# Optimization experiments

Measured on AMD Instinct MI355X. Metric: run time of the kernel, lower is better.

Reference implementation:

```python
import jax, jax.numpy as jnp
import numpy as np

B, NA, NB = 2, 2048, 2048
DIM_A, DIM_B = 256, 256
HEADS, DH_A, DH_B = 8, 64, 64
INNER_A, INNER_B = DH_A * HEADS, DH_B * HEADS
EPS = 1e-5


def layer_norm(x, w, b):
    m = jnp.mean(x, axis=-1, keepdims=True)
    v = jnp.mean(jnp.square(x - m), axis=-1, keepdims=True)
    return (x - m) * jax.lax.rsqrt(v + EPS) * w + b


def setup_inputs() -> dict:
    key = jax.random.key(0)
    ks = jax.random.split(key, 16)
    s = 0.02
    return {
        "feat_a": jax.random.normal(ks[0], (B, NA, DIM_A), jnp.float32),
        "feat_b": jax.random.normal(ks[1], (B, NB, DIM_B), jnp.float32),
        "mask_a_b": jax.random.bernoulli(ks[2], 0.5, (B, NA, NB)),
        # linear weights stored (in, out)
        "Wq": jax.random.normal(ks[3], (DIM_A, INNER_B), jnp.float32) * s,
        "bq": jnp.zeros((INNER_B,), jnp.float32),
        "Wk": jax.random.normal(ks[4], (DIM_B, INNER_B), jnp.float32) * s,
        "bk": jnp.zeros((INNER_B,), jnp.float32),
        "Wv": jax.random.normal(ks[5], (DIM_B, INNER_A), jnp.float32) * s,
        "bv": jnp.zeros((INNER_A,), jnp.float32),
        "Wg": jax.random.normal(ks[6], (DIM_A, INNER_A), jnp.float32) * s,
        "bg": jnp.zeros((INNER_A,), jnp.float32),
        "Wo": jax.random.normal(ks[7], (INNER_A, DIM_A), jnp.float32) * s,
        "bo": jnp.zeros((DIM_A,), jnp.float32),
        "ln_a_w": jnp.ones((DIM_A,), jnp.float32),
        "ln_a_b": jnp.zeros((DIM_A,), jnp.float32),
        "ln_b_w": jnp.ones((DIM_B,), jnp.float32),
        "ln_b_b": jnp.zeros((DIM_B,), jnp.float32),
        "qln_w": jnp.ones((INNER_B,), jnp.float32),
        "qln_b": jnp.zeros((INNER_B,), jnp.float32),
        "kln_w": jnp.ones((INNER_B,), jnp.float32),
        "kln_b": jnp.zeros((INNER_B,), jnp.float32),
    }


def reference(feat_a, feat_b, mask_a_b, Wq, bq, Wk, bk, Wv, bv, Wg, bg, Wo, bo,
              ln_a_w, ln_a_b, ln_b_w, ln_b_b, qln_w, qln_b, kln_w, kln_b):
    scale = DH_B ** -0.5
    fa = layer_norm(feat_a, ln_a_w, ln_a_b)            # (b, na, dim_a)
    fb = layer_norm(feat_b, ln_b_w, ln_b_b)            # (b, nb, dim_b)
    q = layer_norm(fa @ Wq + bq, qln_w, qln_b)         # (b, na, inner_b)
    k = layer_norm(fb @ Wk + bk, kln_w, kln_b)         # (b, nb, inner_b)
    v = fb @ Wv + bv                                   # (b, nb, inner_a)
    g = fa @ Wg + bg                                   # (b, na, inner_a)
    q = q.reshape(B, NA, HEADS, DH_B)
    k = k.reshape(B, NB, HEADS, DH_B)
    v = v.reshape(B, NB, HEADS, DH_A)
    g = g.reshape(B, NA, HEADS, DH_A)
    sim = jnp.einsum('bihd,bjhd->bhij', q, k) * scale  # (b, h, na, nb)
    neg = jnp.finfo(sim.dtype).min
    sim = jnp.where(mask_a_b[:, None, :, :], sim, neg)
    attn = jax.nn.softmax(sim, axis=-1)
    out = jnp.einsum('bhij,bjhd->bihd', attn, v)       # (b, na, h, dh_a)
    out = jax.nn.sigmoid(g) * out
    out = out.reshape(B, NA, INNER_A)
    return out @ Wo + bo                               # (b, na, dim_a)
```

## Files before the change

### kernel.cpp

```cpp
#include <hip/hip_runtime.h>
#include <hip/hip_bf16.h>

using bf16 = __hip_bfloat16;
typedef short bf16x8 __attribute__((ext_vector_type(8)));
typedef float f32x4 __attribute__((ext_vector_type(4)));
typedef unsigned short ushort8_t __attribute__((ext_vector_type(8)));
typedef unsigned uint4_t __attribute__((ext_vector_type(4)));
typedef unsigned uint2_t __attribute__((ext_vector_type(2)));
typedef unsigned long long u64;

static constexpr int NA_ = 2048, NB_ = 2048;
static constexpr int H_ = 8, DH_ = 64, INNER_ = 512;
static constexpr int MROWS = 2 * NA_;

#define MFMA32(a, b, c) __builtin_amdgcn_mfma_f32_16x16x32_bf16(a, b, c, 0, 0, 0)

#if __has_builtin(__builtin_amdgcn_exp2f)
#define EXP2(x) __builtin_amdgcn_exp2f(x)
#else
#define EXP2(x) exp2f(x)
#endif

__device__ __forceinline__ unsigned short bfbits(float x) {
  bf16 h = __float2bfloat16(x);
  return __builtin_bit_cast(unsigned short, h);
}
__device__ __forceinline__ float b2f(unsigned short u) {
  unsigned v = ((unsigned)u) << 16;
  return __builtin_bit_cast(float, v);
}

__device__ __forceinline__ unsigned pkbf(float a, float b) {
  unsigned ua = __builtin_bit_cast(unsigned, a) + 0x8000u;
  unsigned ub = __builtin_bit_cast(unsigned, b) + 0x8000u;
#if __has_builtin(__builtin_amdgcn_perm)
  return __builtin_amdgcn_perm(ub, ua, 0x07060302u);
#else
  return (ua >> 16) | (ub & 0xFFFF0000u);
#endif
}

__global__ __launch_bounds__(256) void prep_kernel(
    const float* __restrict__ fa_in, const float* __restrict__ fb_in,
    const float* __restrict__ law, const float* __restrict__ lab,
    const float* __restrict__ lbw, const float* __restrict__ lbb,
    bf16* __restrict__ fa, bf16* __restrict__ fb,
    const float* __restrict__ Wq, const float* __restrict__ Wk,
    const float* __restrict__ Wv, const float* __restrict__ Wg,
    const float* __restrict__ Wo,
    bf16* __restrict__ Wqt, bf16* __restrict__ Wkt,
    bf16* __restrict__ Wvt, bf16* __restrict__ Wgt,
    bf16* __restrict__ Woth, bf16* __restrict__ Wotl,
    const void* __restrict__ maskp, u64* __restrict__ mbits) {
  int blk = blockIdx.x;
  int t = threadIdx.x;
  if (blk < 2048) {
    int row = blk * 4 + (t >> 6);
    int lane = t & 63;
    const float *src, *w, *bb;
    bf16* dst;
    int r;
    if (row < MROWS) { src = fa_in; w = law; bb = lab; dst = fa; r = row; }
    else             { src = fb_in; w = lbw; bb = lbb; dst = fb; r = row - MROWS; }
    float4 x = *(const float4*)(src + (size_t)r * 256 + lane * 4);
    float s  = (x.x + x.y) + (x.z + x.w);
    float s2 = (x.x * x.x + x.y * x.y) + (x.z * x.z + x.w * x.w);
#pragma unroll
    for (int m = 32; m >= 1; m >>= 1) { s += __shfl_xor(s, m); s2 += __shfl_xor(s2, m); }
    float mean = s * (1.0f / 256.0f);
    float var  = s2 * (1.0f / 256.0f) - mean * mean;
    float rstd = rsqrtf(var + 1e-5f);
    float4 wv = *(const float4*)(w + lane * 4);
    float4 bv = *(const float4*)(bb + lane * 4);
    ushort4 o;
    o.x = bfbits((x.x - mean) * rstd * wv.x + bv.x);
    o.y = bfbits((x.y - mean) * rstd * wv.y + bv.y);
    o.z = bfbits((x.z - mean) * rstd * wv.z + bv.z);
    o.w = bfbits((x.w - mean) * rstd * wv.w + bv.w);
    *(ushort4*)(dst + (size_t)r * 256 + lane * 4) = o;
  } else if (blk < 4608) {
    int z = (blk - 2048) >> 9;
    int idx = ((blk - 2048) & 511) * 256 + t;
    if (z < 4) {
      const float* W = (z == 0) ? Wq : (z == 1) ? Wk : (z == 2) ? Wv : Wg;
      bf16* Wt = (z == 0) ? Wqt : (z == 1) ? Wkt : (z == 2) ? Wvt : Wgt;
      int kk = idx >> 9, n = idx & 511;
      Wt[n * 256 + kk] = __float2bfloat16(W[idx]);
    } else {
      int kk = idx >> 8, n = idx & 255;
      float w = Wo[idx];
      bf16 hi = __float2bfloat16(w);
      Woth[n * 512 + kk] = hi;
      Wotl[n * 512 + kk] = __float2bfloat16(w - __bfloat162float(hi));
    }
  } else {
    __shared__ unsigned shf[4];
    const unsigned char* mu = (const unsigned char*)maskp;
    bool nz = ((t & 3) != 0) && (mu[t] != 0);
    u64 bal = __ballot(nz);
    if ((t & 63) == 0) shf[t >> 6] = (bal != 0ull) ? 1u : 0u;
    __syncthreads();
    bool m8 = (shf[0] | shf[1] | shf[2] | shf[3]) != 0;
    int lane = t & 63, wid = t >> 6;
    int lb = blk - 4608;
    for (size_t word = (size_t)lb * 4 + wid; word < 131072; word += 8192) {
      size_t e = word * 64 + lane;
      int v = m8 ? (int)mu[e] : ((const int*)maskp)[e];
      u64 b2 = __ballot(v != 0);
      if (lane == 0) mbits[word] = b2;
    }
  }
}

__global__ __launch_bounds__(256) void gemm4_kernel(
    const bf16* __restrict__ fa, const bf16* __restrict__ fb,
    const bf16* __restrict__ Wqt, const bf16* __restrict__ Wkt,
    const bf16* __restrict__ Wgt, const bf16* __restrict__ Wvt,
    const float* __restrict__ bq, const float* __restrict__ bk,
    const float* __restrict__ bg, const float* __restrict__ bv,
    const float* __restrict__ qlw, const float* __restrict__ qlb,
    const float* __restrict__ klw, const float* __restrict__ klb,
    bf16* __restrict__ qo, bf16* __restrict__ ko,
    bf16* __restrict__ gout, bf16* __restrict__ vout) {
  __shared__ __align__(16) char sm[27648];
  int z = blockIdx.z;
  int t = threadIdx.x, wave = t >> 6, lane = t & 63;
  int lm = lane & 15, quad = lane >> 4, q8 = quad * 8;

// ... 130 lines not shown
        for (int ni = 0; ni < 4; ni++) {
          int nn = n0 + ni * 16 + lm;
          float bvv = bias[nn];
          int mb = m0 + wm + mi * 16 + quad * 4;
#pragma unroll
          for (int r = 0; r < 4; r++)
            gout[(size_t)(mb + r) * 512 + nn] = __float2bfloat16(acc[mi][ni][r] + bvv);
        }
    } else {
      __syncthreads();
      bf16* buf = (bf16*)sm;
#pragma unroll
      for (int mi = 0; mi < 2; mi++)
#pragma unroll
        for (int ni = 0; ni < 4; ni++) {
          int d_local = ni * 16 + lm;
          float bvv = bias[n0 + d_local];
          int j_local = wm + mi * 16 + quad * 4;
#pragma unroll
          for (int r = 0; r < 4; r++)
            buf[d_local * 136 + j_local + r] = __float2bfloat16(acc[mi][ni][r] + bvv);
        }
      __syncthreads();
      int bidx2 = m0 >> 11, j0g = m0 & 2047, hh = n0 >> 6;
      int dl = t >> 2, jseg = (t & 3) * 32;
      bf16* dstrow = vout + (size_t)((bidx2 * 8 + hh) * 64 + dl) * 2048 + j0g + jseg;
#pragma unroll
      for (int c = 0; c < 4; c++)
        *(ushort8_t*)(dstrow + c * 8) = *(const ushort8_t*)(&buf[dl * 136 + jseg + c * 8]);
    }
  }
}

__global__ __launch_bounds__(512, 4) void attn_kernel(
    const bf16* __restrict__ q, const bf16* __restrict__ k,
    const bf16* __restrict__ vt, const bf16* __restrict__ g,
    const u64* __restrict__ mbits,
    bf16* __restrict__ gh, bf16* __restrict__ gl) {
  __shared__ __align__(16) char smem[46592];
  bf16* Qs = (bf16*)smem;
  bf16* KVB = (bf16*)(smem + 9216);
  float* Om = (float*)(smem + 9216);
  float* Lbuf = (float*)(smem + 46080);
  constexpr int BUFE = 2 * 64 * 72;

  int flat = blockIdx.y * 32 + blockIdx.x;
  int bh = (flat & 7) * 2 + (flat >> 8);
  int qt = (flat >> 3) & 31;
  int bidx = bh >> 3, h = bh & 7;
  int i0 = qt * 64;
  int t = threadIdx.x, wave = t >> 6, lane = t & 63;
  int wj = wave >> 2, wi = wave & 3;
  int lm = lane & 15, quad = lane >> 4, q8 = quad * 8;
  int wj32 = wj * 32, wi16 = wi * 16;
  int srow = t >> 3, scg = (t & 7) * 8;

  int sg = srow & 31;
  int ksrow = (srow & 32) + (((sg & 4) << 2) | ((sg & 24) >> 1) | (sg & 3));
  int ksl = ksrow * 72 + scg;
  int vsl = srow * 72 + scg;

  const bf16* kb = k + (size_t)(bidx * NB_) * INNER_ + h * DH_;
  const bf16* vb = vt + (size_t)(bh * DH_) * NB_;
  const bf16* ksrc = kb + (size_t)srow * INNER_ + scg;
  const bf16* vsrc = vb + (size_t)srow * NB_ + scg;

  *(ushort8_t*)(&Qs[srow * 72 + scg]) =
      *(const ushort8_t*)(q + (size_t)(bidx * NA_ + i0 + srow) * INNER_ + h * DH_ + scg);

  ushort8_t kr = *(const ushort8_t*)(ksrc);
  ushort8_t vr = *(const ushort8_t*)(vsrc);

  __syncthreads();
  bf16x8 bq0 = *(const bf16x8*)(&Qs[(wi16 + lm) * 72 + q8]);
  bf16x8 bq1 = *(const bf16x8*)(&Qs[(wi16 + lm) * 72 + 32 + q8]);

  *(ushort8_t*)(&KVB[ksl]) = kr;
  *(ushort8_t*)(&KVB[64 * 72 + vsl]) = vr;
  kr = *(const ushort8_t*)(ksrc + 64 * INNER_);
  vr = *(const ushort8_t*)(vsrc + 64);

  bf16x8 bone;
  {
    short onev = (lm == 0) ? (short)0x3F80 : (short)0;
#pragma unroll
    for (int i = 0; i < 8; i++) bone[i] = onev;
  }

  f32x4 oacc[4] = {};
  f32x4 lacc = {};

  const u64* mrp = mbits + (size_t)(bidx * NA_ + i0 + wi16 + lm) * (NB_ / 64);
  int shp = wj32 + quad * 8;
  u64 smw = mrp[0] >> shp;

  __syncthreads();

  for (int it = 0; it < 32; it++) {
    bf16* Ks = KVB + (it & 1) * BUFE;
    bf16* Vs = Ks + 64 * 72;
    if (it < 31) {
      bf16* Kn = KVB + ((it + 1) & 1) * BUFE;
      *(ushort8_t*)(&Kn[ksl]) = kr;
      *(ushort8_t*)(&Kn[64 * 72 + vsl]) = vr;
    }
    if (it < 30) {
      kr = *(const ushort8_t*)(ksrc + (size_t)(it + 2) * (64 * INNER_));
      vr = *(const ushort8_t*)(vsrc + (it + 2) * 64);
    }
    u64 nm = (it < 31) ? (mrp[it + 1] >> shp) : 0;

    bf16x8 a00 = *(const bf16x8*)(&Ks[(wj32 + lm) * 72 + q8]);
    bf16x8 a01 = *(const bf16x8*)(&Ks[(wj32 + lm) * 72 + 32 + q8]);
    bf16x8 a10 = *(const bf16x8*)(&Ks[(wj32 + 16 + lm) * 72 + q8]);
    bf16x8 a11 = *(const bf16x8*)(&Ks[(wj32 + 16 + lm) * 72 + 32 + q8]);
    f32x4 st0 = {0.f, 0.f, 0.f, 0.f}, st1 = {0.f, 0.f, 0.f, 0.f};
    st0 = MFMA32(a00, bq0, st0);
    st0 = MFMA32(a01, bq1, st0);
    st1 = MFMA32(a10, bq0, st1);
    st1 = MFMA32(a11, bq1, st1);

    float p0[4], p1[4];
#pragma unroll
    for (int r = 0; r < 4; r++) {
      bool l0 = (smw >> r) & 1ull;
      bool l1 = (smw >> (4 + r)) & 1ull;
      p0[r] = EXP2(l0 ? st0[r] : -200.0f);
      p1[r] = EXP2(l1 ? st1[r] : -200.0f);
    }

    uint4_t u0;
    u0[0] = pkbf(p0[0], p0[1]);
    u0[1] = pkbf(p0[2], p0[3]);
    u0[2] = pkbf(p1[0], p1[1]);
    u0[3] = pkbf(p1[2], p1[3]);
    bf16x8 pa = __builtin_bit_cast(bf16x8, u0);

#pragma unroll
    for (int c = 0; c < 4; c++) {
      bf16x8 v_ = *(const bf16x8*)(&Vs[(c * 16 + lm) * 72 + wj32 + q8]);
      oacc[c] = MFMA32(pa, v_, oacc[c]);
    }
    lacc = MFMA32(pa, bone, lacc);

    smw = nm;
    __syncthreads();
  }

  if (lm == 0) {
#pragma unroll
    for (int r = 0; r < 4; r++)
      Lbuf[wj * 64 + wi16 + quad * 4 + r] = lacc[r];
  }
  if (wj == 1) {
#pragma unroll
    for (int c = 0; c < 4; c++)
#pragma unroll
      for (int r = 0; r < 4; r++)
        Om[(wi16 + quad * 4 + r) * 66 + c * 16 + lm] = oacc[c][r];
  }
  __syncthreads();
  if (wj == 0) {
#pragma unroll
    for (int c = 0; c < 4; c++)
#pragma unroll
      for (int r = 0; r < 4; r++)
        Om[(wi16 + quad * 4 + r) * 66 + c * 16 + lm] += oacc[c][r];
  }
  __syncthreads();
  {
    int row = wave * 8 + (lane >> 3);
    int col = (lane & 7) * 8;
    float l = Lbuf[row] + Lbuf[64 + row];
    float inv = 1.0f / l;
    size_t idx = (size_t)(bidx * NA_ + i0 + row) * INNER_ + h * DH_ + col;
    ushort8_t gv = *(const ushort8_t*)(g + idx);
    ushort8_t oh, ol;
#pragma unroll
    for (int e = 0; e < 8; e++) {
      float o = Om[row * 66 + col + e];
      float gf = b2f((unsigned short)gv[e]);
      float sig = 1.0f / (1.0f + __expf(-gf));
      float val = o * inv * sig;
      unsigned short hb = bfbits(val);
      oh[e] = hb;
      ol[e] = bfbits(val - b2f(hb));
    }
    *(ushort8_t*)(gh + idx) = oh;
    *(ushort8_t*)(gl + idx) = ol;
  }
}

__global__ __launch_bounds__(256) void gemm_split_kernel(
    const bf16* __restrict__ Ah, const bf16* __restrict__ Al,
    const bf16* __restrict__ Bh, const bf16* __restrict__ Bl,
    const float* __restrict__ bias, float* __restrict__ C) {
  constexpr int K = 512, N = 256;
  __shared__ __align__(16) bf16 Ash[32 * 72];
  __shared__ __align__(16) bf16 Asl[32 * 72];
  __shared__ __align__(16) bf16 Bsh[64 * 72];
  __shared__ __align__(16) bf16 Bsl[64 * 72];
  int n0 = blockIdx.x * 64, m0 = blockIdx.y * 32;
  int t = threadIdx.x, wave = t >> 6, lane = t & 63;
  int lm = lane & 15, quad = lane >> 4, q8 = quad * 8;
  int wm = (wave & 1) * 16, wn = (wave >> 1) * 32;
  f32x4 acc[2] = {};
  for (int k0 = 0; k0 < K; k0 += 64) {
    __syncthreads();
    {
      int r = t >> 3, cg = t & 7;
      size_t ga = (size_t)(m0 + r) * K + k0 + cg * 8;
      *(ushort8_t*)(&Ash[r * 72 + cg * 8]) = *(const ushort8_t*)(Ah + ga);
      *(ushort8_t*)(&Asl[r * 72 + cg * 8]) = *(const ushort8_t*)(Al + ga);
    }
#pragma unroll
    for (int i = 0; i < 2; i++) {
      int id = t + 256 * i, r = id >> 3, cg = id & 7;
      size_t gb = (size_t)(n0 + r) * K + k0 + cg * 8;
      *(ushort8_t*)(&Bsh[r * 72 + cg * 8]) = *(const ushort8_t*)(Bh + gb);
      *(ushort8_t*)(&Bsl[r * 72 + cg * 8]) = *(const ushort8_t*)(Bl + gb);
    }
    __syncthreads();
// ... 38 lines not shown
  const float* Wo = (const float*)d_in[11];
  const float* bo = (const float*)d_in[12];
  const float* law = (const float*)d_in[13];
  const float* lab = (const float*)d_in[14];
  const float* lbw = (const float*)d_in[15];
  const float* lbb = (const float*)d_in[16];
  const float* qlw = (const float*)d_in[17];
  const float* qlb = (const float*)d_in[18];
  const float* klw = (const float*)d_in[19];
  const float* klb = (const float*)d_in[20];

  char* ws = (char*)d_ws;
  size_t off = 0;
  auto alloc = [&](size_t bytes) -> void* {
    void* p = ws + off;
    off += (bytes + 255) & ~(size_t)255;
    return p;
  };
  bf16* fa    = (bf16*)alloc((size_t)MROWS * 256 * 2);
  bf16* fb    = (bf16*)alloc((size_t)MROWS * 256 * 2);
  bf16* Wqt   = (bf16*)alloc((size_t)131072 * 2);
  bf16* Wkt   = (bf16*)alloc((size_t)131072 * 2);
  bf16* Wvt   = (bf16*)alloc((size_t)131072 * 2);
  bf16* Wgt   = (bf16*)alloc((size_t)131072 * 2);
  bf16* Woth  = (bf16*)alloc((size_t)131072 * 2);
  bf16* Wotl  = (bf16*)alloc((size_t)131072 * 2);
  bf16* qb_   = (bf16*)alloc((size_t)MROWS * 512 * 2);
  bf16* kb_   = (bf16*)alloc((size_t)MROWS * 512 * 2);
  bf16* vtb   = (bf16*)alloc((size_t)1024 * 2048 * 2);
  bf16* gbuf  = (bf16*)alloc((size_t)MROWS * 512 * 2);
  bf16* gh    = (bf16*)alloc((size_t)MROWS * 512 * 2);
  bf16* gl    = (bf16*)alloc((size_t)MROWS * 512 * 2);
  u64*  mbits = (u64*)alloc((size_t)131072 * 8);

  prep_kernel<<<6656, 256, 0, stream>>>(
      feat_a, feat_b, law, lab, lbw, lbb, fa, fb,
      Wq, Wk, Wv, Wg, Wo, Wqt, Wkt, Wvt, Wgt, Woth, Wotl, mask, mbits);
  gemm4_kernel<<<dim3(256, 1, 4), 256, 0, stream>>>(
      fa, fb, Wqt, Wkt, Wgt, Wvt, bq, bk, bg, bv,
      qlw, qlb, klw, klb, qb_, kb_, gbuf, vtb);
  attn_kernel<<<dim3(32, 16), 512, 0, stream>>>(qb_, kb_, vtb, gbuf, mbits, gh, gl);
  gemm_split_kernel<<<dim3(4, 128), 256, 0, stream>>>(gh, gl, Woth, Wotl, bo, (float*)d_out);
}
```

Measured before the change: 189.2 us.

## Split attention over key halves with flag-based partial combine

The attention kernel now splits the key/value range into two halves across a third grid dimension, doubling the block count. Each block drops from 8 to 4 waves, and every wave now covers 32 query rows instead of 16, which reuses each K/V fragment across two row tiles. Each block writes partial O and L sums to global scratch and bumps an atomic counter per (head, query tile). The block that arrives second combines both halves and applies the gate and bf16 hi/lo split. This aims for more parallelism and better register reuse, at the cost of extra global traffic, a threadfence-based handoff, and flags that the prep kernel must reset on every launch.

```diff
diff --git a/kernel.cpp b/kernel.cpp
--- a/kernel.cpp
+++ b/kernel.cpp
@@ -6,7 +6,6 @@
 typedef float f32x4 __attribute__((ext_vector_type(4)));
 typedef unsigned short ushort8_t __attribute__((ext_vector_type(8)));
 typedef unsigned uint4_t __attribute__((ext_vector_type(4)));
-typedef unsigned uint2_t __attribute__((ext_vector_type(2)));
 typedef unsigned long long u64;
 
 static constexpr int NA_ = 2048, NB_ = 2048;
@@ -51,7 +50,8 @@
     bf16* __restrict__ Wqt, bf16* __restrict__ Wkt,
     bf16* __restrict__ Wvt, bf16* __restrict__ Wgt,
     bf16* __restrict__ Woth, bf16* __restrict__ Wotl,
-    const void* __restrict__ maskp, u64* __restrict__ mbits) {
+    const void* __restrict__ maskp, u64* __restrict__ mbits,
+    unsigned* __restrict__ flags) {
   int blk = blockIdx.x;
   int t = threadIdx.x;
   if (blk < 2048) {
@@ -94,6 +94,7 @@
       Wotl[n * 512 + kk] = __float2bfloat16(w - __bfloat162float(hi));
     }
   } else {
+    if (blk - 4608 < 2) flags[(blk - 4608) * 256 + t] = 0u;
     __shared__ unsigned shf[4];
     const unsigned char* mu = (const unsigned char*)maskp;
     bool nz = ((t & 3) != 0) && (mu[t] != 0);
@@ -290,53 +291,51 @@
   }
 }
 
-__global__ __launch_bounds__(512, 4) void attn_kernel(
+__global__ __launch_bounds__(256, 4) void attn_kernel(
     const bf16* __restrict__ q, const bf16* __restrict__ k,
     const bf16* __restrict__ vt, const bf16* __restrict__ g,
     const u64* __restrict__ mbits,
+    float* __restrict__ opart, float* __restrict__ lpart,
+    unsigned* __restrict__ flags,
     bf16* __restrict__ gh, bf16* __restrict__ gl) {
-  __shared__ __align__(16) char smem[46592];
-  bf16* Qs = (bf16*)smem;
-  bf16* KVB = (bf16*)(smem + 9216);
-  float* Om = (float*)(smem + 9216);
-  float* Lbuf = (float*)(smem + 46080);
+  __shared__ __align__(16) char smem[37408];
+  bf16* KVB = (bf16*)smem;
+  float* Om = (float*)smem;
+  float* Lbuf = (float*)(smem + 36864);
+  unsigned* sflag = (unsigned*)(smem + 37376);
   constexpr int BUFE = 2 * 64 * 72;
 
-  int flat = blockIdx.y * 32 + blockIdx.x;
-  int bh = (flat & 7) * 2 + (flat >> 8);
-  int qt = (flat >> 3) & 31;
+  int fid = blockIdx.x + 32 * blockIdx.y + 512 * blockIdx.z;
+  int bh = (fid & 7) * 2 + ((fid >> 3) & 1);
+  int qt = (fid >> 4) & 31;
+  int jh = fid >> 9;
   int bidx = bh >> 3, h = bh & 7;
   int i0 = qt * 64;
+  int pair = bh * 32 + qt;
   int t = threadIdx.x, wave = t >> 6, lane = t & 63;
-  int wj = wave >> 2, wi = wave & 3;
+  int wj = wave >> 1, wi = wave & 1;
   int lm = lane & 15, quad = lane >> 4, q8 = quad * 8;
-  int wj32 = wj * 32, wi16 = wi * 16;
+  int wj32 = wj * 32, wi32 = wi * 32;
   int srow = t >> 3, scg = (t & 7) * 8;
 
-  int sg = srow & 31;
-  int ksrow = (srow & 32) + (((sg & 4) << 2) | ((sg & 24) >> 1) | (sg & 3));
-  int ksl = ksrow * 72 + scg;
-  int vsl = srow * 72 + scg;
+  int ksrow = ((srow & 4) << 2) | ((srow & 24) >> 1) | (srow & 3);
+  int ksl0 = ksrow * 72 + scg;
+  int ksl1 = (ksrow + 32) * 72 + scg;
+  int vsl0 = srow * 72 + scg;
+  int vsl1 = (srow + 32) * 72 + scg;
 
   const bf16* kb = k + (size_t)(bidx * NB_) * INNER_ + h * DH_;
   const bf16* vb = vt + (size_t)(bh * DH_) * NB_;
-  const bf16* ksrc = kb + (size_t)srow * INNER_ + scg;
-  const bf16* vsrc = vb + (size_t)srow * NB_ + scg;
-
-  *(ushort8_t*)(&Qs[srow * 72 + scg]) =
-      *(const ushort8_t*)(q + (size_t)(bidx * NA_ + i0 + srow) * INNER_ + h * DH_ + scg);
-
-  ushort8_t kr = *(const ushort8_t*)(ksrc);
-  ushort8_t vr = *(const ushort8_t*)(vsrc);
-
-  __syncthreads();
-  bf16x8 bq0 = *(const bf16x8*)(&Qs[(wi16 + lm) * 72 + q8]);
-  bf16x8 bq1 = *(const bf16x8*)(&Qs[(wi16 + lm) * 72 + 32 + q8]);
-
-  *(ushort8_t*)(&KVB[ksl]) = kr;
-  *(ushort8_t*)(&KVB[64 * 72 + vsl]) = vr;
-  kr = *(const ushort8_t*)(ksrc + 64 * INNER_);
-  vr = *(const ushort8_t*)(vsrc + 64);
+  const bf16* ksrc0 = kb + (size_t)(jh * 1024 + srow) * INNER_ + scg;
+  const bf16* ksrc1 = kb + (size_t)(jh * 1024 + srow + 32) * INNER_ + scg;
+  const bf16* vsrc0 = vb + (size_t)srow * NB_ + jh * 1024 + scg;
+  const bf16* vsrc1 = vb + (size_t)(srow + 32) * NB_ + jh * 1024 + scg;
+
+  const bf16* qbase = q + (size_t)(bidx * NA_ + i0 + wi32 + lm) * INNER_ + h * DH_;
+  bf16x8 bq00 = *(const bf16x8*)(qbase + q8);
+  bf16x8 bq01 = *(const bf16x8*)(qbase + 32 + q8);
+  bf16x8 bq10 = *(const bf16x8*)(qbase + 16 * INNER_ + q8);
+  bf16x8 bq11 = *(const bf16x8*)(qbase + 16 * INNER_ + 32 + q8);
 
   bf16x8 bone;
   {
@@ -345,107 +344,177 @@
     for (int i = 0; i < 8; i++) bone[i] = onev;
   }
 
-  f32x4 oacc[4] = {};
-  f32x4 lacc = {};
-
-  const u64* mrp = mbits + (size_t)(bidx * NA_ + i0 + wi16 + lm) * (NB_ / 64);
+  f32x4 oacc[2][4] = {};
+  f32x4 lacc[2] = {};
+
+  const u64* mrp0 = mbits + (size_t)(bidx * NA_ + i0 + wi32 + lm) * (NB_ / 64) + jh * 16;
+  const u64* mrp1 = mrp0 + (size_t)16 * (NB_ / 64);
   int shp = wj32 + quad * 8;
-  u64 smw = mrp[0] >> shp;
-
+
+  ushort8_t kr0 = *(const ushort8_t*)(ksrc0);
+  ushort8_t kr1 = *(const ushort8_t*)(ksrc1);
+  ushort8_t vr0 = *(const ushort8_t*)(vsrc0);
+  ushort8_t vr1 = *(const ushort8_t*)(vsrc1);
+  *(ushort8_t*)(&KVB[ksl0]) = kr0;
+  *(ushort8_t*)(&KVB[ksl1]) = kr1;
+  *(ushort8_t*)(&KVB[64 * 72 + vsl0]) = vr0;
+  *(ushort8_t*)(&KVB[64 * 72 + vsl1]) = vr1;
+  kr0 = *(const ushort8_t*)(ksrc0 + 64 * INNER_);
+  kr1 = *(const ushort8_t*)(ksrc1 + 64 * INNER_);
+  vr0 = *(const ushort8_t*)(vsrc0 + 64);
+  vr1 = *(const ushort8_t*)(vsrc1 + 64);
+  u64 smw0 = mrp0[0] >> shp;
+  u64 smw1 = mrp1[0] >> shp;
   __syncthreads();
 
-  for (int it = 0; it < 32; it++) {
+  for (int it = 0; it < 16; it++) {
     bf16* Ks = KVB + (it & 1) * BUFE;
     bf16* Vs = Ks + 64 * 72;
-    if (it < 31) {
+    if (it < 15) {
       bf16* Kn = KVB + ((it + 1) & 1) * BUFE;
-      *(ushort8_t*)(&Kn[ksl]) = kr;
-      *(ushort8_t*)(&Kn[64 * 72 + vsl]) = vr;
-    }
-    if (it < 30) {
-      kr = *(const ushort8_t*)(ksrc + (size_t)(it + 2) * (64 * INNER_));
-      vr = *(const ushort8_t*)(vsrc + (it + 2) * 64);
-    }
-    u64 nm = (it < 31) ? (mrp[it + 1] >> shp) : 0;
+      *(ushort8_t*)(&Kn[ksl0]) = kr0;
+      *(ushort8_t*)(&Kn[ksl1]) = kr1;
+      *(ushort8_t*)(&Kn[64 * 72 + vsl0]) = vr0;
+      *(ushort8_t*)(&Kn[64 * 72 + vsl1]) = vr1;
+    }
+    if (it < 14) {
+      kr0 = *(const ushort8_t*)(ksrc0 + (size_t)(it + 2) * (64 * INNER_));
+      kr1 = *(const ushort8_t*)(ksrc1 + (size_t)(it + 2) * (64 * INNER_));
+      vr0 = *(const ushort8_t*)(vsrc0 + (it + 2) * 64);
+      vr1 = *(const ushort8_t*)(vsrc1 + (it + 2) * 64);
+    }
+    u64 nm0 = smw0, nm1 = smw1;
+    if (it < 15) {
+      nm0 = mrp0[it + 1] >> shp;
+      nm1 = mrp1[it + 1] >> shp;
+    }
 
     bf16x8 a00 = *(const bf16x8*)(&Ks[(wj32 + lm) * 72 + q8]);
     bf16x8 a01 = *(const bf16x8*)(&Ks[(wj32 + lm) * 72 + 32 + q8]);
     bf16x8 a10 = *(const bf16x8*)(&Ks[(wj32 + 16 + lm) * 72 + q8]);
     bf16x8 a11 = *(const bf16x8*)(&Ks[(wj32 + 16 + lm) * 72 + 32 + q8]);
-    f32x4 st0 = {0.f, 0.f, 0.f, 0.f}, st1 = {0.f, 0.f, 0.f, 0.f};
-    st0 = MFMA32(a00, bq0, st0);
-    st0 = MFMA32(a01, bq1, st0);
-    st1 = MFMA32(a10, bq0, st1);
-    st1 = MFMA32(a11, bq1, st1);
-
-    float p0[4], p1[4];
+    f32x4 st00 = {0.f, 0.f, 0.f, 0.f}, st01 = {0.f, 0.f, 0.f, 0.f};
+    f32x4 st10 = {0.f, 0.f, 0.f, 0.f}, st11 = {0.f, 0.f, 0.f, 0.f};
+    st00 = MFMA32(a00, bq00, st00); st00 = MFMA32(a01, bq01, st00);
+    st01 = MFMA32(a10, bq00, st01); st01 = MFMA32(a11, bq01, st01);
+    st10 = MFMA32(a00, bq10, st10); st10 = MFMA32(a01, bq11, st10);
+    st11 = MFMA32(a10, bq10, st11); st11 = MFMA32(a11, bq11, st11);
+
+    float p00[4], p01[4], p10[4], p11[4];
 #pragma unroll
     for (int r = 0; r < 4; r++) {
-      bool l0 = (smw >> r) & 1ull;
-      bool l1 = (smw >> (4 + r)) & 1ull;
-      p0[r] = EXP2(l0 ? st0[r] : -200.0f);
-      p1[r] = EXP2(l1 ? st1[r] : -200.0f);
-    }
-
-    uint4_t u0;
-    u0[0] = pkbf(p0[0], p0[1]);
-    u0[1] = pkbf(p0[2], p0[3]);
-    u0[2] = pkbf(p1[0], p1[1]);
-    u0[3] = pkbf(p1[2], p1[3]);
-    bf16x8 pa = __builtin_bit_cast(bf16x8, u0);
+      p00[r] = EXP2(((smw0 >> r) & 1ull) ? st00[r] : -200.0f);
+      p01[r] = EXP2(((smw0 >> (4 + r)) & 1ull) ? st01[r] : -200.0f);
+      p10[r] = EXP2(((smw1 >> r) & 1ull) ? st10[r] : -200.0f);
+      p11[r] = EXP2(((smw1 >> (4 + r)) & 1ull) ? st11[r] : -200.0f);
+    }
+
+    uint4_t u0, u1;
+    u0[0] = pkbf(p00[0], p00[1]);
+    u0[1] = pkbf(p00[2], p00[3]);
+    u0[2] = pkbf(p01[0], p01[1]);
+    u0[3] = pkbf(p01[2], p01[3]);
+    u1[0] = pkbf(p10[0], p10[1]);
+    u1[1] = pkbf(p10[2], p10[3]);
+    u1[2] = pkbf(p11[0], p11[1]);
+    u1[3] = pkbf(p11[2], p11[3]);
+    bf16x8 pa0 = __builtin_bit_cast(bf16x8, u0);
+    bf16x8 pa1 = __builtin_bit_cast(bf16x8, u1);
 
 #pragma unroll
     for (int c = 0; c < 4; c++) {
       bf16x8 v_ = *(const bf16x8*)(&Vs[(c * 16 + lm) * 72 + wj32 + q8]);
-      oacc[c] = MFMA32(pa, v_, oacc[c]);
-    }
-    lacc = MFMA32(pa, bone, lacc);
-
-    smw = nm;
+      oacc[0][c] = MFMA32(pa0, v_, oacc[0][c]);
+      oacc[1][c] = MFMA32(pa1, v_, oacc[1][c]);
+    }
+    lacc[0] = MFMA32(pa0, bone, lacc[0]);
+    lacc[1] = MFMA32(pa1, bone, lacc[1]);
+
+    smw0 = nm0;
+    smw1 = nm1;
     __syncthreads();
   }
 
   if (lm == 0) {
 #pragma unroll
-    for (int r = 0; r < 4; r++)
-      Lbuf[wj * 64 + wi16 + quad * 4 + r] = lacc[r];
+    for (int is_ = 0; is_ < 2; is_++)
+#pragma unroll
+      for (int r = 0; r < 4; r++)
+        Lbuf[wj * 64 + wi32 + is_ * 16 + quad * 4 + r] = lacc[is_][r];
   }
   if (wj == 1) {
 #pragma unroll
-    for (int c = 0; c < 4; c++)
-#pragma unroll
-      for (int r = 0; r < 4; r++)
-        Om[(wi16 + quad * 4 + r) * 66 + c * 16 + lm] = oacc[c][r];
+    for (int is_ = 0; is_ < 2; is_++)
+#pragma unroll
+      for (int c = 0; c < 4; c++)
+#pragma unroll
+        for (int r = 0; r < 4; r++)
+          Om[(wi32 + is_ * 16 + quad * 4 + r) * 66 + c * 16 + lm] = oacc[is_][c][r];
   }
   __syncthreads();
   if (wj == 0) {
 #pragma unroll
-    for (int c = 0; c < 4; c++)
-#pragma unroll
-      for (int r = 0; r < 4; r++)
-        Om[(wi16 + quad * 4 + r) * 66 + c * 16 + lm] += oacc[c][r];
+    for (int is_ = 0; is_ < 2; is_++)
+#pragma unroll
+      for (int c = 0; c < 4; c++)
+#pragma unroll
+        for (int r = 0; r < 4; r++)
+          Om[(wi32 + is_ * 16 + quad * 4 + r) * 66 + c * 16 + lm] += oacc[is_][c][r];
   }
   __syncthreads();
+
+  int slot = pair * 2 + jh;
   {
-    int row = wave * 8 + (lane >> 3);
-    int col = (lane & 7) * 8;
-    float l = Lbuf[row] + Lbuf[64 + row];
+    int row = t >> 2, c0 = (t & 3) * 16;
+    float* dst = opart + (size_t)slot * 4096 + row * 64 + c0;
+#pragma unroll
+    for (int e = 0; e < 4; e++) {
+      float4 v4 = *(float4*)(&Om[row * 66 + c0 + e * 4]);
+      *(float4*)(dst + e * 4) = v4;
+    }
+    if (t < 64) lpart[slot * 64 + t] = Lbuf[t] + Lbuf[64 + t];
+  }
+  __syncthreads();
+  __threadfence();
+  if (t == 0) *sflag = atomicAdd(&flags[pair], 1u);
+  __syncthreads();
+  if (*sflag == 0) return;
+  __threadfence();
+
+  {
+    int pslot = pair * 2 + (1 - jh);
+    int row = t >> 2, c0 = (t & 3) * 16;
+    const float* psrc = opart + (size_t)pslot * 4096 + row * 64 + c0;
+    float l = Lbuf[row] + Lbuf[64 + row] + lpart[pslot * 64 + row];
     float inv = 1.0f / l;
-    size_t idx = (size_t)(bidx * NA_ + i0 + row) * INNER_ + h * DH_ + col;
-    ushort8_t gv = *(const ushort8_t*)(g + idx);
-    ushort8_t oh, ol;
+    size_t idx = (size_t)(bidx * NA_ + i0 + row) * INNER_ + h * DH_ + c0;
+    ushort8_t gv0 = *(const ushort8_t*)(g + idx);
+    ushort8_t gv1 = *(const ushort8_t*)(g + idx + 8);
+    ushort8_t oh0, ol0, oh1, ol1;
 #pragma unroll
     for (int e = 0; e < 8; e++) {
-      float o = Om[row * 66 + col + e];
-      float gf = b2f((unsigned short)gv[e]);
+      float o = Om[row * 66 + c0 + e] + psrc[e];
+      float gf = b2f((unsigned short)gv0[e]);
       float sig = 1.0f / (1.0f + __expf(-gf));
       float val = o * inv * sig;
       unsigned short hb = bfbits(val);
-      oh[e] = hb;
-      ol[e] = bfbits(val - b2f(hb));
-    }
-    *(ushort8_t*)(gh + idx) = oh;
-    *(ushort8_t*)(gl + idx) = ol;
+      oh0[e] = hb;
+      ol0[e] = bfbits(val - b2f(hb));
+    }
+#pragma unroll
+    for (int e = 0; e < 8; e++) {
+      float o = Om[row * 66 + c0 + 8 + e] + psrc[8 + e];
+      float gf = b2f((unsigned short)gv1[e]);
+      float sig = 1.0f / (1.0f + __expf(-gf));
+      float val = o * inv * sig;
+      unsigned short hb = bfbits(val);
+      oh1[e] = hb;
+      ol1[e] = bfbits(val - b2f(hb));
+    }
+    *(ushort8_t*)(gh + idx) = oh0;
+    *(ushort8_t*)(gh + idx + 8) = oh1;
+    *(ushort8_t*)(gl + idx) = ol0;
+    *(ushort8_t*)(gl + idx + 8) = ol1;
   }
 }
 
@@ -550,13 +619,17 @@
   bf16* gh    = (bf16*)alloc((size_t)MROWS * 512 * 2);
   bf16* gl    = (bf16*)alloc((size_t)MROWS * 512 * 2);
   u64*  mbits = (u64*)alloc((size_t)131072 * 8);
+  float* opart = (float*)alloc((size_t)1024 * 4096 * 4);
+  float* lpart = (float*)alloc((size_t)1024 * 64 * 4);
+  unsigned* flags = (unsigned*)alloc((size_t)512 * 4);
 
   prep_kernel<<<6656, 256, 0, stream>>>(
       feat_a, feat_b, law, lab, lbw, lbb, fa, fb,
-      Wq, Wk, Wv, Wg, Wo, Wqt, Wkt, Wvt, Wgt, Woth, Wotl, mask, mbits);
+      Wq, Wk, Wv, Wg, Wo, Wqt, Wkt, Wvt, Wgt, Woth, Wotl, mask, mbits, flags);
   gemm4_kernel<<<dim3(256, 1, 4), 256, 0, stream>>>(
       fa, fb, Wqt, Wkt, Wgt, Wvt, bq, bk, bg, bv,
       qlw, qlb, klw, klb, qb_, kb_, gbuf, vtb);
-  attn_kernel<<<dim3(32, 16), 512, 0, stream>>>(qb_, kb_, vtb, gbuf, mbits, gh, gl);
+  attn_kernel<<<dim3(32, 16, 2), 256, 0, stream>>>(
+      qb_, kb_, vtb, gbuf, mbits, opart, lpart, flags, gh, gl);
   gemm_split_kernel<<<dim3(4, 128), 256, 0, stream>>>(gh, gl, Woth, Wotl, bo, (float*)d_out);
 }
```

New measurement: 397.4 us. 110% more time.

## Retile attention so each wave covers 32 query rows across two key-tile halves

Applied to the files above, without the earlier changes.

Each wave now handles two 16-row query blocks instead of one, reusing the same K and V fragments from shared memory for both. The 8 waves split into 2 query halves, 2 key halves and 2 key-tile groups, and each iteration stages two 64-key K/V tiles. This halves the loop trip count and the number of barriers, and Q fragments are now loaded straight from global into registers. In exchange, shared memory grows to about 73 KB, register pressure rises from the doubled accumulators, and the final reduction across four wave groups needs more serialized barrier steps. Occupancy per CU may drop.

```diff
diff --git a/kernel.cpp b/kernel.cpp
--- a/kernel.cpp
+++ b/kernel.cpp
@@ -6,7 +6,6 @@
 typedef float f32x4 __attribute__((ext_vector_type(4)));
 typedef unsigned short ushort8_t __attribute__((ext_vector_type(8)));
 typedef unsigned uint4_t __attribute__((ext_vector_type(4)));
-typedef unsigned uint2_t __attribute__((ext_vector_type(2)));
 typedef unsigned long long u64;
 
 static constexpr int NA_ = 2048, NB_ = 2048;
@@ -295,12 +294,12 @@
     const bf16* __restrict__ vt, const bf16* __restrict__ g,
     const u64* __restrict__ mbits,
     bf16* __restrict__ gh, bf16* __restrict__ gl) {
-  __shared__ __align__(16) char smem[46592];
-  bf16* Qs = (bf16*)smem;
-  bf16* KVB = (bf16*)(smem + 9216);
-  float* Om = (float*)(smem + 9216);
-  float* Lbuf = (float*)(smem + 46080);
-  constexpr int BUFE = 2 * 64 * 72;
+  __shared__ __align__(16) char smem[74752];
+  bf16* KVB = (bf16*)smem;
+  float* Om = (float*)smem;
+  float* Lbuf = (float*)(smem + 73728);
+  constexpr int TILE = 64 * 72;
+  constexpr int BUFE = 4 * TILE;
 
   int flat = blockIdx.y * 32 + blockIdx.x;
   int bh = (flat & 7) * 2 + (flat >> 8);
@@ -308,9 +307,9 @@
   int bidx = bh >> 3, h = bh & 7;
   int i0 = qt * 64;
   int t = threadIdx.x, wave = t >> 6, lane = t & 63;
-  int wj = wave >> 2, wi = wave & 3;
+  int wi = wave & 1, wj = (wave >> 1) & 1, jh = wave >> 2;
   int lm = lane & 15, quad = lane >> 4, q8 = quad * 8;
-  int wj32 = wj * 32, wi16 = wi * 16;
+  int wj32 = wj * 32, wi32 = wi * 32;
   int srow = t >> 3, scg = (t & 7) * 8;
 
   int sg = srow & 31;
@@ -323,20 +322,11 @@
   const bf16* ksrc = kb + (size_t)srow * INNER_ + scg;
   const bf16* vsrc = vb + (size_t)srow * NB_ + scg;
 
-  *(ushort8_t*)(&Qs[srow * 72 + scg]) =
-      *(const ushort8_t*)(q + (size_t)(bidx * NA_ + i0 + srow) * INNER_ + h * DH_ + scg);
-
-  ushort8_t kr = *(const ushort8_t*)(ksrc);
-  ushort8_t vr = *(const ushort8_t*)(vsrc);
-
-  __syncthreads();
-  bf16x8 bq0 = *(const bf16x8*)(&Qs[(wi16 + lm) * 72 + q8]);
-  bf16x8 bq1 = *(const bf16x8*)(&Qs[(wi16 + lm) * 72 + 32 + q8]);
-
-  *(ushort8_t*)(&KVB[ksl]) = kr;
-  *(ushort8_t*)(&KVB[64 * 72 + vsl]) = vr;
-  kr = *(const ushort8_t*)(ksrc + 64 * INNER_);
-  vr = *(const ushort8_t*)(vsrc + 64);
+  const bf16* qbase = q + (size_t)(bidx * NA_ + i0 + wi32 + lm) * INNER_ + h * DH_;
+  bf16x8 bq00 = *(const bf16x8*)(qbase + q8);
+  bf16x8 bq01 = *(const bf16x8*)(qbase + 32 + q8);
+  bf16x8 bq10 = *(const bf16x8*)(qbase + 16 * INNER_ + q8);
+  bf16x8 bq11 = *(const bf16x8*)(qbase + 16 * INNER_ + 32 + q8);
 
   bf16x8 bone;
   {
@@ -345,91 +335,151 @@
     for (int i = 0; i < 8; i++) bone[i] = onev;
   }
 
-  f32x4 oacc[4] = {};
-  f32x4 lacc = {};
-
-  const u64* mrp = mbits + (size_t)(bidx * NA_ + i0 + wi16 + lm) * (NB_ / 64);
+  f32x4 oacc[2][4] = {};
+  f32x4 lacc[2] = {};
+
+  const u64* mrp0 = mbits + (size_t)(bidx * NA_ + i0 + wi32 + lm) * (NB_ / 64);
+  const u64* mrp1 = mrp0 + (size_t)16 * (NB_ / 64);
   int shp = wj32 + quad * 8;
-  u64 smw = mrp[0] >> shp;
-
+
+  ushort8_t kra = *(const ushort8_t*)(ksrc);
+  ushort8_t krb = *(const ushort8_t*)(ksrc + (size_t)64 * INNER_);
+  ushort8_t vra = *(const ushort8_t*)(vsrc);
+  ushort8_t vrb = *(const ushort8_t*)(vsrc + 64);
+  *(ushort8_t*)(&KVB[ksl]) = kra;
+  *(ushort8_t*)(&KVB[TILE + vsl]) = vra;
+  *(ushort8_t*)(&KVB[2 * TILE + ksl]) = krb;
+  *(ushort8_t*)(&KVB[3 * TILE + vsl]) = vrb;
+  kra = *(const ushort8_t*)(ksrc + (size_t)128 * INNER_);
+  krb = *(const ushort8_t*)(ksrc + (size_t)192 * INNER_);
+  vra = *(const ushort8_t*)(vsrc + 128);
+  vrb = *(const ushort8_t*)(vsrc + 192);
+  u64 smw0 = mrp0[jh] >> shp;
+  u64 smw1 = mrp1[jh] >> shp;
   __syncthreads();
 
-  for (int it = 0; it < 32; it++) {
-    bf16* Ks = KVB + (it & 1) * BUFE;
-    bf16* Vs = Ks + 64 * 72;
-    if (it < 31) {
-      bf16* Kn = KVB + ((it + 1) & 1) * BUFE;
-      *(ushort8_t*)(&Kn[ksl]) = kr;
-      *(ushort8_t*)(&Kn[64 * 72 + vsl]) = vr;
-    }
-    if (it < 30) {
-      kr = *(const ushort8_t*)(ksrc + (size_t)(it + 2) * (64 * INNER_));
-      vr = *(const ushort8_t*)(vsrc + (it + 2) * 64);
-    }
-    u64 nm = (it < 31) ? (mrp[it + 1] >> shp) : 0;
+  for (int it = 0; it < 16; it++) {
+    bf16* buf = KVB + (it & 1) * BUFE;
+    bf16* Ks = buf + jh * (2 * TILE);
+    bf16* Vs = Ks + TILE;
+    if (it < 15) {
+      bf16* nb = KVB + ((it + 1) & 1) * BUFE;
+      *(ushort8_t*)(&nb[ksl]) = kra;
+      *(ushort8_t*)(&nb[TILE + vsl]) = vra;
+      *(ushort8_t*)(&nb[2 * TILE + ksl]) = krb;
+      *(ushort8_t*)(&nb[3 * TILE + vsl]) = vrb;
+    }
+    if (it < 14) {
+      int T = (it + 2) * 2;
+      kra = *(const ushort8_t*)(ksrc + (size_t)T * (64 * INNER_));
+      krb = *(const ushort8_t*)(ksrc + (size_t)(T + 1) * (64 * INNER_));
+      vra = *(const ushort8_t*)(vsrc + T * 64);
+      vrb = *(const ushort8_t*)(vsrc + (T + 1) * 64);
+    }
+    u64 nm0 = smw0, nm1 = smw1;
+    if (it < 15) {
+      nm0 = mrp0[(it + 1) * 2 + jh] >> shp;
+      nm1 = mrp1[(it + 1) * 2 + jh] >> shp;
+    }
 
     bf16x8 a00 = *(const bf16x8*)(&Ks[(wj32 + lm) * 72 + q8]);
     bf16x8 a01 = *(const bf16x8*)(&Ks[(wj32 + lm) * 72 + 32 + q8]);
     bf16x8 a10 = *(const bf16x8*)(&Ks[(wj32 + 16 + lm) * 72 + q8]);
     bf16x8 a11 = *(const bf16x8*)(&Ks[(wj32 + 16 + lm) * 72 + 32 + q8]);
-    f32x4 st0 = {0.f, 0.f, 0.f, 0.f}, st1 = {0.f, 0.f, 0.f, 0.f};
-    st0 = MFMA32(a00, bq0, st0);
-    st0 = MFMA32(a01, bq1, st0);
-    st1 = MFMA32(a10, bq0, st1);
-    st1 = MFMA32(a11, bq1, st1);
-
-    float p0[4], p1[4];
+    f32x4 st00 = {0.f, 0.f, 0.f, 0.f}, st01 = {0.f, 0.f, 0.f, 0.f};
+    f32x4 st10 = {0.f, 0.f, 0.f, 0.f}, st11 = {0.f, 0.f, 0.f, 0.f};
+    st00 = MFMA32(a00, bq00, st00); st00 = MFMA32(a01, bq01, st00);
+    st01 = MFMA32(a10, bq00, st01); st01 = MFMA32(a11, bq01, st01);
+    st10 = MFMA32(a00, bq10, st10); st10 = MFMA32(a01, bq11, st10);
+    st11 = MFMA32(a10, bq10, st11); st11 = MFMA32(a11, bq11, st11);
+
+    float p00[4], p01[4], p10[4], p11[4];
 #pragma unroll
     for (int r = 0; r < 4; r++) {
-      bool l0 = (smw >> r) & 1ull;
-      bool l1 = (smw >> (4 + r)) & 1ull;
-      p0[r] = EXP2(l0 ? st0[r] : -200.0f);
-      p1[r] = EXP2(l1 ? st1[r] : -200.0f);
-    }
-
-    uint4_t u0;
-    u0[0] = pkbf(p0[0], p0[1]);
-    u0[1] = pkbf(p0[2], p0[3]);
-    u0[2] = pkbf(p1[0], p1[1]);
-    u0[3] = pkbf(p1[2], p1[3]);
-    bf16x8 pa = __builtin_bit_cast(bf16x8, u0);
+      p00[r] = EXP2(((smw0 >> r) & 1ull) ? st00[r] : -200.0f);
+      p01[r] = EXP2(((smw0 >> (4 + r)) & 1ull) ? st01[r] : -200.0f);
+      p10[r] = EXP2(((smw1 >> r) & 1ull) ? st10[r] : -200.0f);
+      p11[r] = EXP2(((smw1 >> (4 + r)) & 1ull) ? st11[r] : -200.0f);
+    }
+
+    uint4_t u0, u1;
+    u0[0] = pkbf(p00[0], p00[1]);
+    u0[1] = pkbf(p00[2], p00[3]);
+    u0[2] = pkbf(p01[0], p01[1]);
+    u0[3] = pkbf(p01[2], p01[3]);
+    u1[0] = pkbf(p10[0], p10[1]);
+    u1[1] = pkbf(p10[2], p10[3]);
+    u1[2] = pkbf(p11[0], p11[1]);
+    u1[3] = pkbf(p11[2], p11[3]);
+    bf16x8 pa0 = __builtin_bit_cast(bf16x8, u0);
+    bf16x8 pa1 = __builtin_bit_cast(bf16x8, u1);
 
 #pragma unroll
     for (int c = 0; c < 4; c++) {
       bf16x8 v_ = *(const bf16x8*)(&Vs[(c * 16 + lm) * 72 + wj32 + q8]);
-      oacc[c] = MFMA32(pa, v_, oacc[c]);
-    }
-    lacc = MFMA32(pa, bone, lacc);
-
-    smw = nm;
+      oacc[0][c] = MFMA32(pa0, v_, oacc[0][c]);
+      oacc[1][c] = MFMA32(pa1, v_, oacc[1][c]);
+    }
+    lacc[0] = MFMA32(pa0, bone, lacc[0]);
+    lacc[1] = MFMA32(pa1, bone, lacc[1]);
+
+    smw0 = nm0;
+    smw1 = nm1;
     __syncthreads();
   }
 
+  int grp = jh * 2 + wj;
   if (lm == 0) {
 #pragma unroll
-    for (int r = 0; r < 4; r++)
-      Lbuf[wj * 64 + wi16 + quad * 4 + r] = lacc[r];
-  }
-  if (wj == 1) {
-#pragma unroll
-    for (int c = 0; c < 4; c++)
+    for (int is_ = 0; is_ < 2; is_++)
 #pragma unroll
       for (int r = 0; r < 4; r++)
-        Om[(wi16 + quad * 4 + r) * 66 + c * 16 + lm] = oacc[c][r];
+        Lbuf[grp * 64 + wi32 + is_ * 16 + quad * 4 + r] = lacc[is_][r];
+  }
+  if (grp == 3) {
+#pragma unroll
+    for (int is_ = 0; is_ < 2; is_++)
+#pragma unroll
+      for (int c = 0; c < 4; c++)
+#pragma unroll
+        for (int r = 0; r < 4; r++)
+          Om[(wi32 + is_ * 16 + quad * 4 + r) * 66 + c * 16 + lm] = oacc[is_][c][r];
   }
   __syncthreads();
-  if (wj == 0) {
-#pragma unroll
-    for (int c = 0; c < 4; c++)
-#pragma unroll
-      for (int r = 0; r < 4; r++)
-        Om[(wi16 + quad * 4 + r) * 66 + c * 16 + lm] += oacc[c][r];
+  if (grp == 2) {
+#pragma unroll
+    for (int is_ = 0; is_ < 2; is_++)
+#pragma unroll
+      for (int c = 0; c < 4; c++)
+#pragma unroll
+        for (int r = 0; r < 4; r++)
+          Om[(wi32 + is_ * 16 + quad * 4 + r) * 66 + c * 16 + lm] += oacc[is_][c][r];
+  }
+  __syncthreads();
+  if (grp == 1) {
+#pragma unroll
+    for (int is_ = 0; is_ < 2; is_++)
+#pragma unroll
+      for (int c = 0; c < 4; c++)
+#pragma unroll
+        for (int r = 0; r < 4; r++)
+          Om[(wi32 + is_ * 16 + quad * 4 + r) * 66 + c * 16 + lm] += oacc[is_][c][r];
+  }
+  __syncthreads();
+  if (grp == 0) {
+#pragma unroll
+    for (int is_ = 0; is_ < 2; is_++)
+#pragma unroll
+      for (int c = 0; c < 4; c++)
+#pragma unroll
+        for (int r = 0; r < 4; r++)
+          Om[(wi32 + is_ * 16 + quad * 4 + r) * 66 + c * 16 + lm] += oacc[is_][c][r];
   }
   __syncthreads();
   {
-    int row = wave * 8 + (lane >> 3);
-    int col = (lane & 7) * 8;
-    float l = Lbuf[row] + Lbuf[64 + row];
+    int row = t >> 3;
+    int col = (t & 7) * 8;
+    float l = Lbuf[row] + Lbuf[64 + row] + Lbuf[128 + row] + Lbuf[192 + row];
     float inv = 1.0f / l;
     size_t idx = (size_t)(bidx * NA_ + i0 + row) * INNER_ + h * DH_ + col;
     ushort8_t gv = *(const ushort8_t*)(g + idx);
```

Result: slower. 196.2 us (+3.7%).

## Software-pipeline attention loop: defer PV MFMAs one iteration, load Q directly

Applied to the files above, without the earlier changes.

Restructures the attention main loop so the P·V and row-sum MFMAs for the previous key tile run at the start of the next iteration. This lets them overlap with the QK^T MFMAs and the exp/pack work, and the V fragments are held in registers across the barrier. Q fragments are now read straight from global memory into registers instead of being staged through shared memory, which drops the Q shared buffer and one barrier and shrinks LDS use. In exchange the kernel holds more live registers (carried P and V fragments), which could hurt occupancy at 512 threads.

```diff
diff --git a/kernel.cpp b/kernel.cpp
--- a/kernel.cpp
+++ b/kernel.cpp
@@ -6,7 +6,6 @@
 typedef float f32x4 __attribute__((ext_vector_type(4)));
 typedef unsigned short ushort8_t __attribute__((ext_vector_type(8)));
 typedef unsigned uint4_t __attribute__((ext_vector_type(4)));
-typedef unsigned uint2_t __attribute__((ext_vector_type(2)));
 typedef unsigned long long u64;
 
 static constexpr int NA_ = 2048, NB_ = 2048;
@@ -295,12 +294,12 @@
     const bf16* __restrict__ vt, const bf16* __restrict__ g,
     const u64* __restrict__ mbits,
     bf16* __restrict__ gh, bf16* __restrict__ gl) {
-  __shared__ __align__(16) char smem[46592];
-  bf16* Qs = (bf16*)smem;
-  bf16* KVB = (bf16*)(smem + 9216);
-  float* Om = (float*)(smem + 9216);
-  float* Lbuf = (float*)(smem + 46080);
-  constexpr int BUFE = 2 * 64 * 72;
+  __shared__ __align__(16) char smem[37376];
+  bf16* KVB = (bf16*)smem;
+  float* Om = (float*)smem;
+  float* Lbuf = (float*)(smem + 36864);
+  constexpr int TILE = 64 * 72;
+  constexpr int BUFE = 2 * TILE;
 
   int flat = blockIdx.y * 32 + blockIdx.x;
   int bh = (flat & 7) * 2 + (flat >> 8);
@@ -316,27 +315,16 @@
   int sg = srow & 31;
   int ksrow = (srow & 32) + (((sg & 4) << 2) | ((sg & 24) >> 1) | (sg & 3));
   int ksl = ksrow * 72 + scg;
-  int vsl = srow * 72 + scg;
+  int vsl = TILE + srow * 72 + scg;
 
   const bf16* kb = k + (size_t)(bidx * NB_) * INNER_ + h * DH_;
   const bf16* vb = vt + (size_t)(bh * DH_) * NB_;
   const bf16* ksrc = kb + (size_t)srow * INNER_ + scg;
   const bf16* vsrc = vb + (size_t)srow * NB_ + scg;
 
-  *(ushort8_t*)(&Qs[srow * 72 + scg]) =
-      *(const ushort8_t*)(q + (size_t)(bidx * NA_ + i0 + srow) * INNER_ + h * DH_ + scg);
-
-  ushort8_t kr = *(const ushort8_t*)(ksrc);
-  ushort8_t vr = *(const ushort8_t*)(vsrc);
-
-  __syncthreads();
-  bf16x8 bq0 = *(const bf16x8*)(&Qs[(wi16 + lm) * 72 + q8]);
-  bf16x8 bq1 = *(const bf16x8*)(&Qs[(wi16 + lm) * 72 + 32 + q8]);
-
-  *(ushort8_t*)(&KVB[ksl]) = kr;
-  *(ushort8_t*)(&KVB[64 * 72 + vsl]) = vr;
-  kr = *(const ushort8_t*)(ksrc + 64 * INNER_);
-  vr = *(const ushort8_t*)(vsrc + 64);
+  const bf16* qbase = q + (size_t)(bidx * NA_ + i0 + wi16 + lm) * INNER_ + h * DH_;
+  bf16x8 bq0 = *(const bf16x8*)(qbase + q8);
+  bf16x8 bq1 = *(const bf16x8*)(qbase + 32 + q8);
 
   bf16x8 bone;
   {
@@ -350,23 +338,27 @@
 
   const u64* mrp = mbits + (size_t)(bidx * NA_ + i0 + wi16 + lm) * (NB_ / 64);
   int shp = wj32 + quad * 8;
+
+  ushort8_t kr = *(const ushort8_t*)(ksrc);
+  ushort8_t vr = *(const ushort8_t*)(vsrc);
+  *(ushort8_t*)(&KVB[ksl]) = kr;
+  *(ushort8_t*)(&KVB[vsl]) = vr;
+  kr = *(const ushort8_t*)(ksrc + (size_t)64 * INNER_);
+  vr = *(const ushort8_t*)(vsrc + 64);
   u64 smw = mrp[0] >> shp;
-
   __syncthreads();
 
-  for (int it = 0; it < 32; it++) {
-    bf16* Ks = KVB + (it & 1) * BUFE;
-    bf16* Vs = Ks + 64 * 72;
-    if (it < 31) {
-      bf16* Kn = KVB + ((it + 1) & 1) * BUFE;
-      *(ushort8_t*)(&Kn[ksl]) = kr;
-      *(ushort8_t*)(&Kn[64 * 72 + vsl]) = vr;
-    }
-    if (it < 30) {
-      kr = *(const ushort8_t*)(ksrc + (size_t)(it + 2) * (64 * INNER_));
-      vr = *(const ushort8_t*)(vsrc + (it + 2) * 64);
-    }
-    u64 nm = (it < 31) ? (mrp[it + 1] >> shp) : 0;
+  bf16x8 paP, vP0, vP1, vP2, vP3;
+
+  {
+    bf16* Ks = KVB;
+    bf16* Vs = KVB + TILE;
+    bf16* Kn = KVB + BUFE;
+    *(ushort8_t*)(&Kn[ksl]) = kr;
+    *(ushort8_t*)(&Kn[vsl]) = vr;
+    kr = *(const ushort8_t*)(ksrc + (size_t)128 * INNER_);
+    vr = *(const ushort8_t*)(vsrc + 128);
+    u64 nm = mrp[1] >> shp;
 
     bf16x8 a00 = *(const bf16x8*)(&Ks[(wj32 + lm) * 72 + q8]);
     bf16x8 a01 = *(const bf16x8*)(&Ks[(wj32 + lm) * 72 + 32 + q8]);
@@ -381,29 +373,83 @@
     float p0[4], p1[4];
 #pragma unroll
     for (int r = 0; r < 4; r++) {
-      bool l0 = (smw >> r) & 1ull;
-      bool l1 = (smw >> (4 + r)) & 1ull;
-      p0[r] = EXP2(l0 ? st0[r] : -200.0f);
-      p1[r] = EXP2(l1 ? st1[r] : -200.0f);
-    }
-
+      p0[r] = EXP2(((smw >> r) & 1ull) ? st0[r] : -200.0f);
+      p1[r] = EXP2(((smw >> (4 + r)) & 1ull) ? st1[r] : -200.0f);
+    }
     uint4_t u0;
     u0[0] = pkbf(p0[0], p0[1]);
     u0[1] = pkbf(p0[2], p0[3]);
     u0[2] = pkbf(p1[0], p1[1]);
     u0[3] = pkbf(p1[2], p1[3]);
-    bf16x8 pa = __builtin_bit_cast(bf16x8, u0);
-
-#pragma unroll
-    for (int c = 0; c < 4; c++) {
-      bf16x8 v_ = *(const bf16x8*)(&Vs[(c * 16 + lm) * 72 + wj32 + q8]);
-      oacc[c] = MFMA32(pa, v_, oacc[c]);
-    }
-    lacc = MFMA32(pa, bone, lacc);
+    paP = __builtin_bit_cast(bf16x8, u0);
+
+    vP0 = *(const bf16x8*)(&Vs[(0 * 16 + lm) * 72 + wj32 + q8]);
+    vP1 = *(const bf16x8*)(&Vs[(1 * 16 + lm) * 72 + wj32 + q8]);
+    vP2 = *(const bf16x8*)(&Vs[(2 * 16 + lm) * 72 + wj32 + q8]);
+    vP3 = *(const bf16x8*)(&Vs[(3 * 16 + lm) * 72 + wj32 + q8]);
 
     smw = nm;
     __syncthreads();
   }
+
+  for (int it = 1; it < 32; it++) {
+    bf16* Ks = KVB + (it & 1) * BUFE;
+    bf16* Vs = Ks + TILE;
+    if (it < 31) {
+      bf16* Kn = KVB + ((it + 1) & 1) * BUFE;
+      *(ushort8_t*)(&Kn[ksl]) = kr;
+      *(ushort8_t*)(&Kn[vsl]) = vr;
+    }
+    if (it < 30) {
+      kr = *(const ushort8_t*)(ksrc + (size_t)(it + 2) * (64 * INNER_));
+      vr = *(const ushort8_t*)(vsrc + (it + 2) * 64);
+    }
+    u64 nm = (it < 31) ? (mrp[it + 1] >> shp) : 0;
+
+    oacc[0] = MFMA32(paP, vP0, oacc[0]);
+    oacc[1] = MFMA32(paP, vP1, oacc[1]);
+    oacc[2] = MFMA32(paP, vP2, oacc[2]);
+    oacc[3] = MFMA32(paP, vP3, oacc[3]);
+    lacc = MFMA32(paP, bone, lacc);
+
+    bf16x8 a00 = *(const bf16x8*)(&Ks[(wj32 + lm) * 72 + q8]);
+    bf16x8 a01 = *(const bf16x8*)(&Ks[(wj32 + lm) * 72 + 32 + q8]);
+    bf16x8 a10 = *(const bf16x8*)(&Ks[(wj32 + 16 + lm) * 72 + q8]);
+    bf16x8 a11 = *(const bf16x8*)(&Ks[(wj32 + 16 + lm) * 72 + 32 + q8]);
+    f32x4 st0 = {0.f, 0.f, 0.f, 0.f}, st1 = {0.f, 0.f, 0.f, 0.f};
+    st0 = MFMA32(a00, bq0, st0);
+    st0 = MFMA32(a01, bq1, st0);
+    st1 = MFMA32(a10, bq0, st1);
+    st1 = MFMA32(a11, bq1, st1);
+
+    bf16x8 vC0 = *(const bf16x8*)(&Vs[(0 * 16 + lm) * 72 + wj32 + q8]);
+    bf16x8 vC1 = *(const bf16x8*)(&Vs[(1 * 16 + lm) * 72 + wj32 + q8]);
+    bf16x8 vC2 = *(const bf16x8*)(&Vs[(2 * 16 + lm) * 72 + wj32 + q8]);
+    bf16x8 vC3 = *(const bf16x8*)(&Vs[(3 * 16 + lm) * 72 + wj32 + q8]);
+
+    float p0[4], p1[4];
+#pragma unroll
+    for (int r = 0; r < 4; r++) {
+      p0[r] = EXP2(((smw >> r) & 1ull) ? st0[r] : -200.0f);
+      p1[r] = EXP2(((smw >> (4 + r)) & 1ull) ? st1[r] : -200.0f);
+    }
+    uint4_t u0;
+    u0[0] = pkbf(p0[0], p0[1]);
+    u0[1] = pkbf(p0[2], p0[3]);
+    u0[2] = pkbf(p1[0], p1[1]);
+    u0[3] = pkbf(p1[2], p1[3]);
+    paP = __builtin_bit_cast(bf16x8, u0);
+    vP0 = vC0; vP1 = vC1; vP2 = vC2; vP3 = vC3;
+
+    smw = nm;
+    __syncthreads();
+  }
+
+  oacc[0] = MFMA32(paP, vP0, oacc[0]);
+  oacc[1] = MFMA32(paP, vP1, oacc[1]);
+  oacc[2] = MFMA32(paP, vP2, oacc[2]);
+  oacc[3] = MFMA32(paP, vP3, oacc[3]);
+  lacc = MFMA32(paP, bone, lacc);
 
   if (lm == 0) {
 #pragma unroll
```

New measurement: 191.6 us. Within noise of the previous version (+1.2%).
